# Optimization experiments

Hardware: AMD Instinct MI355X
Metric: run time of the kernel (lower is better)

## Reference

```python
import jax, jax.numpy as jnp
import numpy as np

N_NODES = 200000
N_EDGES = 5000000
N_GRAPHS = 1024
HID = 16
ALPHA = 0.2


def _sage_conv(x, src, dst, Wl, bl, Wr):
    # PyG SAGEConv(aggr='mean'): out = lin_l(mean_{j->i} x_j) + lin_r(x_i)
    msg = x[src]                                                  # [E, d] gather
    summed = jax.ops.segment_sum(msg, dst, num_segments=N_NODES)  # [N, d]
    deg = jax.ops.segment_sum(jnp.ones((src.shape[0],), x.dtype), dst, num_segments=N_NODES)
    mean = summed / jnp.maximum(deg, 1.0)[:, None]
    return mean @ Wl + bl + x @ Wr


def _attention_pool(x, batch):
    scores = jnp.exp(ALPHA * x)                                   # [N, d]
    denom = jax.ops.segment_sum(scores, batch, num_segments=N_GRAPHS)
    scores = scores / denom[batch]
    return jax.ops.segment_sum(x * scores, batch, num_segments=N_GRAPHS)  # [B, d]


def setup_inputs() -> dict:
    key = jax.random.key(0)
    ks = jax.random.split(key, 32)
    inp = {}
    inp['x'] = jax.random.normal(ks[0], (N_NODES, 1), dtype=jnp.float32)
    inp['edge_index'] = jax.random.randint(ks[1], (2, N_EDGES), 0, N_NODES, dtype=jnp.int32)
    inp['batch'] = jnp.sort(jax.random.randint(ks[2], (N_NODES,), 0, N_GRAPHS, dtype=jnp.int32))
    dims = [(1, HID), (HID, HID), (HID, HID)]
    k = 3
    for i, (di, do) in enumerate(dims):
        inp[f'Wl{i}'] = jax.random.normal(ks[k], (di, do), jnp.float32) * 0.1; k += 1
        inp[f'bl{i}'] = jnp.zeros((do,), jnp.float32)
        inp[f'Wr{i}'] = jax.random.normal(ks[k], (di, do), jnp.float32) * 0.1; k += 1
        inp[f'Wlin{i}'] = jax.random.normal(ks[k], (HID, HID), jnp.float32) * 0.1; k += 1
        inp[f'blin{i}'] = jnp.zeros((HID,), jnp.float32)
    inp['Wo0'] = jax.random.normal(ks[k], (HID, HID), jnp.float32) * 0.1; k += 1
    inp['bo0'] = jnp.zeros((HID,), jnp.float32)
    inp['Wo1'] = jax.random.normal(ks[k], (HID, HID), jnp.float32) * 0.1; k += 1
    inp['bo1'] = jnp.zeros((HID,), jnp.float32)
    inp['Wo2'] = jax.random.normal(ks[k], (HID, 1), jnp.float32) * 0.1; k += 1
    inp['bo2'] = jnp.zeros((1,), jnp.float32)
    return inp


def reference(x, edge_index, batch,
              Wl0, bl0, Wr0, Wlin0, blin0,
              Wl1, bl1, Wr1, Wlin1, blin1,
              Wl2, bl2, Wr2, Wlin2, blin2,
              Wo0, bo0, Wo1, bo1, Wo2, bo2):
    src, dst = edge_index[0], edge_index[1]
    Wls = [Wl0, Wl1, Wl2]; bls = [bl0, bl1, bl2]; Wrs = [Wr0, Wr1, Wr2]
    Wlins = [Wlin0, Wlin1, Wlin2]; blins = [blin0, blin1, blin2]
    for i in range(3):
        x = jax.nn.relu(_sage_conv(x, src, dst, Wls[i], bls[i], Wrs[i]))
        x = x @ Wlins[i] + blins[i]
    x = _attention_pool(x, batch)                                 # [B, HID]
    x = jax.nn.relu(x @ Wo0 + bo0)
    x = jax.nn.relu(x @ Wo1 + bo1)
    return x @ Wo2 + bo2                                          # [B, 1]
```

## Files before the change

kernel.cpp:

```cpp
#include <hip/hip_runtime.h>

#define N_NODES 200000
#define N_EDGES 5000000
#define N_GRAPHS 1024
#define HID 16
#define ALPHA 0.2f

#define BSH 7
#define BSZ 128
#define NB 1563
#define NWGB 256
#define EPB ((N_EDGES + NWGB - 1) / NWGB)

#define SACCP 20

__global__ void count_kernel(const int* __restrict__ dst, int* __restrict__ M) {
    __shared__ int hist[NB];
    for (int i = threadIdx.x; i < NB; i += 256) hist[i] = 0;
    __syncthreads();
    int base = blockIdx.x * EPB;
    int end = min(base + EPB, N_EDGES);
    for (int e = base + threadIdx.x; e < end; e += 256)
        atomicAdd(&hist[dst[e] >> BSH], 1);
    __syncthreads();
    for (int i = threadIdx.x; i < NB; i += 256)
        M[i * NWGB + blockIdx.x] = hist[i];
}

__global__ void colscan_kernel(int* __restrict__ M, int* __restrict__ col_total) {
    int b = blockIdx.x * blockDim.x + threadIdx.x;
    if (b >= NB) return;
    int* row = M + b * NWGB;
    int run = 0;
#pragma unroll 8
    for (int w = 0; w < NWGB; ++w) { int v = row[w]; row[w] = run; run += v; }
    col_total[b] = run;
}

__global__ void bucketscan_kernel(const int* __restrict__ col_total,
                                  int* __restrict__ bucket_base) {
    __shared__ int sc[256];
    int t = threadIdx.x;
    int v[7];
    int s = 0;
#pragma unroll
    for (int k = 0; k < 7; ++k) {
        int i = t * 7 + k;
        v[k] = (i < NB) ? col_total[i] : 0;
        s += v[k];
    }
    sc[t] = s;
    __syncthreads();
    for (int off = 1; off < 256; off <<= 1) {
        int tmp = (t >= off) ? sc[t - off] : 0;
        __syncthreads();
        sc[t] += tmp;
        __syncthreads();
    }
    int excl = sc[t] - s;
#pragma unroll
    for (int k = 0; k < 7; ++k) {
        int i = t * 7 + k;
        if (i < NB) bucket_base[i] = excl;
        excl += v[k];
    }
    if (t == 255) bucket_base[NB] = sc[255];
}

__global__ void scatter_build_kernel(const int* __restrict__ src,
                                     const int* __restrict__ dst,
                                     const int* __restrict__ M,
                                     const int* __restrict__ bucket_base,
                                     int* __restrict__ packed) {
    __shared__ int cur[NB];
    int w = blockIdx.x;
    for (int i = threadIdx.x; i < NB; i += 256)
        cur[i] = bucket_base[i] + M[i * NWGB + w];
    __syncthreads();
    int base = w * EPB;
    int end = min(base + EPB, N_EDGES);
    for (int e = base + threadIdx.x; e < end; e += 256) {
        int s = src[e], d = dst[e];
        int p = atomicAdd(&cur[d >> BSH], 1);
        packed[p] = (s << BSH) | (d & (BSZ - 1));
    }
}

__global__ void csr_kernel(const int* __restrict__ packed,
                           const int* __restrict__ bucket_base,
                           int* __restrict__ row_ptr,
                           int* __restrict__ sorted_src) {
    __shared__ int cnt[BSZ], scn[BSZ], cur[BSZ];
    int t = threadIdx.x, b = blockIdx.x;
    if (t < BSZ) cnt[t] = 0;
    __syncthreads();
    int e0 = bucket_base[b], e1 = bucket_base[b + 1];
    for (int i = e0 + t; i < e1; i += 256)
        atomicAdd(&cnt[packed[i] & (BSZ - 1)], 1);
    __syncthreads();
    if (t < BSZ) scn[t] = cnt[t];
    __syncthreads();
    for (int off = 1; off < BSZ; off <<= 1) {
        int v = 0;
        if (t < BSZ && t >= off) v = scn[t - off];
        __syncthreads();
        if (t < BSZ) scn[t] += v;
        __syncthreads();
    }
    if (t < BSZ) {
        int node = b * BSZ + t;
        int base = e0 + scn[t] - cnt[t];
        if (node < N_NODES) row_ptr[node] = base;
        cur[t] = base;
    }
    if (b == NB - 1 && t == 0) row_ptr[N_NODES] = N_EDGES;
    __syncthreads();
    for (int i = e0 + t; i < e1; i += 256) {
        int pk = packed[i];
        int p = atomicAdd(&cur[pk & (BSZ - 1)], 1);
        sorted_src[p] = pk >> BSH;
    }
}

__global__ void layer0_csr(const float* __restrict__ x,
                           const int* __restrict__ row_ptr,
                           const int* __restrict__ sorted_src,
                           const float* __restrict__ Wl, const float* __restrict__ bl,
                           const float* __restrict__ Wr,
                           const float* __restrict__ Wlin, const float* __restrict__ blin,
                           float* __restrict__ xout) {
    __shared__ float sWl[HID], sWr[HID], sbl[HID], sblin[HID], sWlin[HID * HID];
    int t = threadIdx.x;
    if (t < HID) {
        sWl[t] = Wl[t]; sWr[t] = Wr[t]; sbl[t] = bl[t]; sblin[t] = blin[t];
    }
    if (t < HID * HID) sWlin[t] = Wlin[t];
    __syncthreads();

    int n = blockIdx.x * 256 + t;
    if (n >= N_NODES) return;
    int r0 = row_ptr[n], r1 = row_ptr[n + 1];
    float sum = 0.0f;
    int i = r0;
    for (; i + 4 <= r1; i += 4) {
        int s0 = sorted_src[i], s1 = sorted_src[i + 1];
        int s2 = sorted_src[i + 2], s3 = sorted_src[i + 3];
        sum += x[s0] + x[s1] + x[s2] + x[s3];
    }
    for (; i < r1; ++i) sum += x[sorted_src[i]];
    float mean = sum / fmaxf((float)(r1 - r0), 1.0f);
    float xv = x[n];
    float h[HID];
#pragma unroll
    for (int j = 0; j < HID; ++j)
        h[j] = fmaxf(mean * sWl[j] + sbl[j] + xv * sWr[j], 0.0f);
    float o[HID];
#pragma unroll
    for (int j = 0; j < HID; ++j) {
        float a = sblin[j];
#pragma unroll
        for (int k = 0; k < HID; ++k) a += h[k] * sWlin[k * HID + j];
        o[j] = a;
    }
    float4* op = reinterpret_cast<float4*>(xout + (size_t)n * HID);
#pragma unroll
    for (int q = 0; q < 4; ++q)
        op[q] = make_float4(o[q * 4 + 0], o[q * 4 + 1], o[q * 4 + 2], o[q * 4 + 3]);
}

__global__ void layerB_csr(const float* __restrict__ xin,
                           const int* __restrict__ row_ptr,
                           const int* __restrict__ sorted_src,
                           const float* __restrict__ Wl, const float* __restrict__ bl,
                           const float* __restrict__ Wr,
                           const float* __restrict__ Wlin, const float* __restrict__ blin,
                           float* __restrict__ xout) {
    __shared__ float sacc[64 * SACCP];
    __shared__ float sxv[64 * SACCP];
    __shared__ float sh[64 * SACCP];
    __shared__ float sWl[HID * HID], sWr[HID * HID], sWlin[HID * HID];
    __shared__ float sbl[HID], sblin[HID];
    int t = threadIdx.x;
    if (t < HID * HID) { sWl[t] = Wl[t]; sWr[t] = Wr[t]; sWlin[t] = Wlin[t]; }
    if (t < HID) { sbl[t] = bl[t]; sblin[t] = blin[t]; }
    __syncthreads();

    int q = t & 3;
    int g = t >> 2;
    int n = blockIdx.x * 64 + g;

    if (n < N_NODES) {
        int r0 = row_ptr[n], r1 = row_ptr[n + 1];
        const float* xq = xin + 4 * q;
        float4 acc = make_float4(0.0f, 0.0f, 0.0f, 0.0f);
        int i = r0;
        for (; i + 4 <= r1; i += 4) {
            int s0 = sorted_src[i], s1 = sorted_src[i + 1];
            int s2 = sorted_src[i + 2], s3 = sorted_src[i + 3];
            float4 g0 = *reinterpret_cast<const float4*>(xq + (size_t)s0 * HID);
            float4 g1 = *reinterpret_cast<const float4*>(xq + (size_t)s1 * HID);
            float4 g2 = *reinterpret_cast<const float4*>(xq + (size_t)s2 * HID);
            float4 g3 = *reinterpret_cast<const float4*>(xq + (size_t)s3 * HID);
            acc.x += g0.x + g1.x + g2.x + g3.x;
            acc.y += g0.y + g1.y + g2.y + g3.y;
            acc.z += g0.z + g1.z + g2.z + g3.z;
            acc.w += g0.w + g1.w + g2.w + g3.w;
        }
        for (; i < r1; ++i) {
            float4 gv = *reinterpret_cast<const float4*>(xq + (size_t)sorted_src[i] * HID);
            acc.x += gv.x; acc.y += gv.y; acc.z += gv.z; acc.w += gv.w;
        }
        float invd = 1.0f / fmaxf((float)(r1 - r0), 1.0f);
        acc.x *= invd; acc.y *= invd; acc.z *= invd; acc.w *= invd;
        *reinterpret_cast<float4*>(&sacc[g * SACCP + 4 * q]) = acc;
        *reinterpret_cast<float4*>(&sxv[g * SACCP + 4 * q]) =
            *reinterpret_cast<const float4*>(xin + (size_t)n * HID + 4 * q);
    }
    __syncthreads();

    if (n < N_NODES) {
        float h4[4];
#pragma unroll
        for (int jj = 0; jj < 4; ++jj) {
            int j = 4 * q + jj;
            float a = sbl[j];
#pragma unroll
            for (int k = 0; k < HID; ++k)
                a += sacc[g * SACCP + k] * sWl[k * HID + j]
                   + sxv[g * SACCP + k] * sWr[k * HID + j];
            h4[jj] = fmaxf(a, 0.0f);
        }
        *reinterpret_cast<float4*>(&sh[g * SACCP + 4 * q]) =
            make_float4(h4[0], h4[1], h4[2], h4[3]);
    }
    __syncthreads();

    if (n < N_NODES) {
        float o4[4];
#pragma unroll
        for (int jj = 0; jj < 4; ++jj) {
            int j = 4 * q + jj;
            float a = sblin[j];
#pragma unroll
            for (int k = 0; k < HID; ++k) a += sh[g * SACCP + k] * sWlin[k * HID + j];
            o4[jj] = a;
        }
        *reinterpret_cast<float4*>(xout + (size_t)n * HID + 4 * q) =
            make_float4(o4[0], o4[1], o4[2], o4[3]);
    }
}

__global__ void scatter0_kernel(const float* __restrict__ x,
                                const int* __restrict__ src,
                                const int* __restrict__ dst,
                                float* __restrict__ sum0,
                                float* __restrict__ deg) {
    int stride = gridDim.x * blockDim.x;
    for (int e = blockIdx.x * blockDim.x + threadIdx.x; e < N_EDGES; e += stride) {
        atomicAdd(&sum0[dst[e]], x[src[e]]);
        atomicAdd(&deg[dst[e]], 1.0f);
    }
}

__global__ void scatter16_kernel(const float* __restrict__ x,
                                 const int* __restrict__ src,
                                 const int* __restrict__ dst,
                                 float* __restrict__ summed) {
    int stride = gridDim.x * blockDim.x;
    const int total = N_EDGES * HID;
    for (int t = blockIdx.x * blockDim.x + threadIdx.x; t < total; t += stride) {
        int e = t >> 4, j = t & 15;
        atomicAdd(&summed[dst[e] * HID + j], x[src[e] * HID + j]);
    }
}

__global__ void node0_kernel(const float* __restrict__ x,
                             const float* __restrict__ sum0,
                             const float* __restrict__ deg,
                             const float* __restrict__ Wl, const float* __restrict__ bl,
                             const float* __restrict__ Wr,
                             const float* __restrict__ Wlin, const float* __restrict__ blin,
                             float* __restrict__ xout) {
    __shared__ float sWl[HID], sWr[HID], sbl[HID], sblin[HID], sWlin[HID * HID];
    if (threadIdx.x < HID) {
        sWl[threadIdx.x] = Wl[threadIdx.x]; sWr[threadIdx.x] = Wr[threadIdx.x];
        sbl[threadIdx.x] = bl[threadIdx.x]; sblin[threadIdx.x] = blin[threadIdx.x];
    }
    if (threadIdx.x < HID * HID) sWlin[threadIdx.x] = Wlin[threadIdx.x];
    __syncthreads();
    int stride = gridDim.x * blockDim.x;
    for (int n = blockIdx.x * blockDim.x + threadIdx.x; n < N_NODES; n += stride) {
        float mean = sum0[n] / fmaxf(deg[n], 1.0f);
        float xv = x[n];
        float h[HID];
#pragma unroll
        for (int j = 0; j < HID; ++j)
            h[j] = fmaxf(mean * sWl[j] + sbl[j] + xv * sWr[j], 0.0f);
#pragma unroll
        for (int j = 0; j < HID; ++j) {
            float acc = sblin[j];
#pragma unroll
            for (int k = 0; k < HID; ++k) acc += h[k] * sWlin[k * HID + j];
            xout[n * HID + j] = acc;
        }
    }
}

__global__ void node16_kernel(const float* __restrict__ xin,
                              const float* __restrict__ sums,
                              const float* __restrict__ deg,
                              const float* __restrict__ Wl, const float* __restrict__ bl,
                              const float* __restrict__ Wr,
                              const float* __restrict__ Wlin, const float* __restrict__ blin,
                              float* __restrict__ xout) {
    __shared__ float sWl[HID * HID], sWr[HID * HID], sWlin[HID * HID];
    __shared__ float sbl[HID], sblin[HID];
    if (threadIdx.x < HID * HID) {
        sWl[threadIdx.x] = Wl[threadIdx.x]; sWr[threadIdx.x] = Wr[threadIdx.x];
        sWlin[threadIdx.x] = Wlin[threadIdx.x];
    }
    if (threadIdx.x < HID) { sbl[threadIdx.x] = bl[threadIdx.x]; sblin[threadIdx.x] = blin[threadIdx.x]; }
    __syncthreads();
    int stride = gridDim.x * blockDim.x;
    for (int n = blockIdx.x * blockDim.x + threadIdx.x; n < N_NODES; n += stride) {
        float invd = 1.0f / fmaxf(deg[n], 1.0f);
        float m[HID], xv[HID];
        const float4* sp = reinterpret_cast<const float4*>(sums + (size_t)n * HID);
        const float4* xp = reinterpret_cast<const float4*>(xin + (size_t)n * HID);
#pragma unroll
        for (int qq = 0; qq < 4; ++qq) {
            float4 sv = sp[qq]; float4 vv = xp[qq];
            m[qq * 4 + 0] = sv.x * invd; m[qq * 4 + 1] = sv.y * invd;
            m[qq * 4 + 2] = sv.z * invd; m[qq * 4 + 3] = sv.w * invd;
            xv[qq * 4 + 0] = vv.x; xv[qq * 4 + 1] = vv.y; xv[qq * 4 + 2] = vv.z; xv[qq * 4 + 3] = vv.w;
        }
        float h[HID];
#pragma unroll
        for (int j = 0; j < HID; ++j) {
            float a = sbl[j];
#pragma unroll
            for (int k = 0; k < HID; ++k) a += m[k] * sWl[k * HID + j];
#pragma unroll
            for (int k = 0; k < HID; ++k) a += xv[k] * sWr[k * HID + j];
            h[j] = fmaxf(a, 0.0f);
        }
        float o[HID];
#pragma unroll
        for (int j = 0; j < HID; ++j) {
            float a = sblin[j];
#pragma unroll
            for (int k = 0; k < HID; ++k) a += h[k] * sWlin[k * HID + j];
            o[j] = a;
        }
        float4* op = reinterpret_cast<float4*>(xout + (size_t)n * HID);
#pragma unroll
        for (int qq = 0; qq < 4; ++qq)
            op[qq] = make_float4(o[qq * 4 + 0], o[qq * 4 + 1], o[qq * 4 + 2], o[qq * 4 + 3]);
    }
}

__global__ void pool_head_kernel(const float* __restrict__ x,
                                 const int* __restrict__ batch,
                                 const float* __restrict__ Wo0, const float* __restrict__ bo0,
                                 const float* __restrict__ Wo1, const float* __restrict__ bo1,
                                 const float* __restrict__ Wo2, const float* __restrict__ bo2,
                                 float* __restrict__ out) {
    int g = blockIdx.x;
    __shared__ int sRange[2];
    __shared__ float red_d[256], red_n[256];
    __shared__ float pooled[HID], h0[HID], h1[HID];

    if (threadIdx.x == 0) {
        int lo = 0, hi = N_NODES;
        while (lo < hi) { int mid = (lo + hi) >> 1; if (batch[mid] < g) lo = mid + 1; else hi = mid; }
        sRange[0] = lo;
        hi = N_NODES;
        while (lo < hi) { int mid = (lo + hi) >> 1; if (batch[mid] < g + 1) lo = mid + 1; else hi = mid; }
        sRange[1] = lo;
    }
    __syncthreads();
    int start = sRange[0], end = sRange[1];
    int j = threadIdx.x & 15;
    int sub = threadIdx.x >> 4;

    float dacc = 0.0f, nacc = 0.0f;
    for (int n = start + sub; n < end; n += 16) {
        float v = x[n * HID + j];
        float s = expf(ALPHA * v);
        dacc += s;
        nacc += s * v;
    }
    red_d[threadIdx.x] = dacc;
    red_n[threadIdx.x] = nacc;
    __syncthreads();

    if (threadIdx.x < HID) {
        float ds = 0.0f, ns = 0.0f;
        for (int k = 0; k < 16; ++k) {
            ds += red_d[k * 16 + threadIdx.x];
            ns += red_n[k * 16 + threadIdx.x];
        }
        pooled[threadIdx.x] = ds > 0.0f ? ns / ds : 0.0f;
    }
    __syncthreads();
    if (threadIdx.x < HID) {
        float acc = bo0[threadIdx.x];
        for (int k = 0; k < HID; ++k) acc += pooled[k] * Wo0[k * HID + threadIdx.x];
        h0[threadIdx.x] = fmaxf(acc, 0.0f);
    }
    __syncthreads();
    if (threadIdx.x < HID) {
        float acc = bo1[threadIdx.x];
        for (int k = 0; k < HID; ++k) acc += h0[k] * Wo1[k * HID + threadIdx.x];
        h1[threadIdx.x] = fmaxf(acc, 0.0f);
    }
    __syncthreads();
    if (threadIdx.x == 0) {
        float acc = bo2[0];
        for (int k = 0; k < HID; ++k) acc += h1[k] * Wo2[k];
        out[g] = acc;
    }
}

extern "C" void kernel_launch(void* const* d_in, const int* in_sizes, int n_in,
                              void* d_out, int out_size, void* d_ws, size_t ws_size,
                              hipStream_t stream) {
    const float* x      = (const float*)d_in[0];
    const int*   edge   = (const int*)d_in[1];
    const int*   batch  = (const int*)d_in[2];
    const float* Wl0    = (const float*)d_in[3];
    const float* bl0    = (const float*)d_in[4];
    const float* Wr0    = (const float*)d_in[5];
    const float* Wlin0  = (const float*)d_in[6];
    const float* blin0  = (const float*)d_in[7];
    const float* Wl1    = (const float*)d_in[8];
    const float* bl1    = (const float*)d_in[9];
    const float* Wr1    = (const float*)d_in[10];
    const float* Wlin1  = (const float*)d_in[11];
    const float* blin1  = (const float*)d_in[12];
    const float* Wl2    = (const float*)d_in[13];
    const float* bl2    = (const float*)d_in[14];
    const float* Wr2    = (const float*)d_in[15];
    const float* Wlin2  = (const float*)d_in[16];
    const float* blin2  = (const float*)d_in[17];
    const float* Wo0    = (const float*)d_in[18];
    const float* bo0    = (const float*)d_in[19];
    const float* Wo1    = (const float*)d_in[20];
    const float* bo1    = (const float*)d_in[21];
    const float* Wo2    = (const float*)d_in[22];
    const float* bo2    = (const float*)d_in[23];

    const int* src = edge;
    const int* dst = edge + N_EDGES;

    const size_t OFF_SORTED = 0;
    const size_t OFF_ROW    = 20000000;
    const size_t OFF_M      = 20800016;
    const size_t OFF_XA     = 22400528;
    const size_t OFF_XB     = 35200528;
    const size_t NEED_MAIN  = 48000528;
    const size_t OFF_PACKED = OFF_XA;
    const size_t OFF_CT     = 42400528;
    const size_t OFF_BB     = 42406800;

    char* ws = (char*)d_ws;

    if (ws_size >= NEED_MAIN) {
        int*   sorted_src  = (int*)(ws + OFF_SORTED);
        int*   row_ptr     = (int*)(ws + OFF_ROW);
        int*   M           = (int*)(ws + OFF_M);
        float* xa          = (float*)(ws + OFF_XA);
        float* xb          = (float*)(ws + OFF_XB);
        int*   packed      = (int*)(ws + OFF_PACKED);
        int*   col_total   = (int*)(ws + OFF_CT);
        int*   bucket_base = (int*)(ws + OFF_BB);

        count_kernel<<<NWGB, 256, 0, stream>>>(dst, M);
        colscan_kernel<<<(NB + 255) / 256, 256, 0, stream>>>(M, col_total);
        bucketscan_kernel<<<1, 256, 0, stream>>>(col_total, bucket_base);
        scatter_build_kernel<<<NWGB, 256, 0, stream>>>(src, dst, M, bucket_base, packed);
        csr_kernel<<<NB, 256, 0, stream>>>(packed, bucket_base, row_ptr, sorted_src);

        layer0_csr<<<(N_NODES + 255) / 256, 256, 0, stream>>>(
            x, row_ptr, sorted_src, Wl0, bl0, Wr0, Wlin0, blin0, xa);
        layerB_csr<<<(N_NODES + 63) / 64, 256, 0, stream>>>(
            xa, row_ptr, sorted_src, Wl1, bl1, Wr1, Wlin1, blin1, xb);
        layerB_csr<<<(N_NODES + 63) / 64, 256, 0, stream>>>(
            xb, row_ptr, sorted_src, Wl2, bl2, Wr2, Wlin2, blin2, xa);

        pool_head_kernel<<<N_GRAPHS, 256, 0, stream>>>(xa, batch, Wo0, bo0, Wo1, bo1,
                                                       Wo2, bo2, (float*)d_out);
    } else {
        float* deg    = (float*)ws;
        float* summed = deg + N_NODES;
        float* xa     = summed + (size_t)N_NODES * HID;
        float* xb     = xa + (size_t)N_NODES * HID;

        hipMemsetAsync(deg, 0, sizeof(float) * (size_t)N_NODES * (1 + HID), stream);
        scatter0_kernel<<<2048, 256, 0, stream>>>(x, src, dst, summed, deg);
        node0_kernel<<<784, 256, 0, stream>>>(x, summed, deg, Wl0, bl0, Wr0, Wlin0, blin0, xa);

        hipMemsetAsync(summed, 0, sizeof(float) * (size_t)N_NODES * HID, stream);
        scatter16_kernel<<<4096, 256, 0, stream>>>(xa, src, dst, summed);
        node16_kernel<<<784, 256, 0, stream>>>(xa, summed, deg, Wl1, bl1, Wr1, Wlin1, blin1, xb);

        hipMemsetAsync(summed, 0, sizeof(float) * (size_t)N_NODES * HID, stream);
        scatter16_kernel<<<4096, 256, 0, stream>>>(xb, src, dst, summed);
        node16_kernel<<<784, 256, 0, stream>>>(xb, summed, deg, Wl2, bl2, Wr2, Wlin2, blin2, xa);

        pool_head_kernel<<<N_GRAPHS, 256, 0, stream>>>(xa, batch, Wo0, bo0, Wo1, bo1,
                                                       Wo2, bo2, (float*)d_out);
    }
}
```

Measured before the change: 533.8 us.

## Fuse layer-0 aggregation into CSR build and vectorize edge histogram passes

```diff
diff --git a/kernel.cpp b/kernel.cpp
--- a/kernel.cpp
+++ b/kernel.cpp
@@ -20,20 +20,28 @@
     __syncthreads();
     int base = blockIdx.x * EPB;
     int end = min(base + EPB, N_EDGES);
-    for (int e = base + threadIdx.x; e < end; e += 256)
-        atomicAdd(&hist[dst[e] >> BSH], 1);
+    for (int e = base + threadIdx.x * 4; e < end; e += 256 * 4) {
+        int4 d4 = *reinterpret_cast<const int4*>(dst + e);
+        atomicAdd(&hist[d4.x >> BSH], 1);
+        atomicAdd(&hist[d4.y >> BSH], 1);
+        atomicAdd(&hist[d4.z >> BSH], 1);
+        atomicAdd(&hist[d4.w >> BSH], 1);
+    }
     __syncthreads();
     for (int i = threadIdx.x; i < NB; i += 256)
-        M[i * NWGB + blockIdx.x] = hist[i];
+        M[blockIdx.x * NB + i] = hist[i];
 }
 
 __global__ void colscan_kernel(int* __restrict__ M, int* __restrict__ col_total) {
     int b = blockIdx.x * blockDim.x + threadIdx.x;
     if (b >= NB) return;
-    int* row = M + b * NWGB;
     int run = 0;
 #pragma unroll 8
-    for (int w = 0; w < NWGB; ++w) { int v = row[w]; row[w] = run; run += v; }
+    for (int w = 0; w < NWGB; ++w) {
+        int v = M[w * NB + b];
+        M[w * NB + b] = run;
+        run += v;
+    }
     col_total[b] = run;
 }
 
@@ -75,28 +83,40 @@
     __shared__ int cur[NB];
     int w = blockIdx.x;
     for (int i = threadIdx.x; i < NB; i += 256)
-        cur[i] = bucket_base[i] + M[i * NWGB + w];
+        cur[i] = bucket_base[i] + M[w * NB + i];
     __syncthreads();
     int base = w * EPB;
     int end = min(base + EPB, N_EDGES);
-    for (int e = base + threadIdx.x; e < end; e += 256) {
-        int s = src[e], d = dst[e];
-        int p = atomicAdd(&cur[d >> BSH], 1);
-        packed[p] = (s << BSH) | (d & (BSZ - 1));
-    }
-}
-
-__global__ void csr_kernel(const int* __restrict__ packed,
+    for (int e = base + threadIdx.x * 4; e < end; e += 256 * 4) {
+        int4 s4 = *reinterpret_cast<const int4*>(src + e);
+        int4 d4 = *reinterpret_cast<const int4*>(dst + e);
+        int p;
+        p = atomicAdd(&cur[d4.x >> BSH], 1); packed[p] = (s4.x << BSH) | (d4.x & (BSZ - 1));
+        p = atomicAdd(&cur[d4.y >> BSH], 1); packed[p] = (s4.y << BSH) | (d4.y & (BSZ - 1));
+        p = atomicAdd(&cur[d4.z >> BSH], 1); packed[p] = (s4.z << BSH) | (d4.z & (BSZ - 1));
+        p = atomicAdd(&cur[d4.w >> BSH], 1); packed[p] = (s4.w << BSH) | (d4.w & (BSZ - 1));
+    }
+}
+
+__global__ void csr_kernel(const float* __restrict__ x,
+                           const int* __restrict__ packed,
                            const int* __restrict__ bucket_base,
                            int* __restrict__ row_ptr,
-                           int* __restrict__ sorted_src) {
+                           int* __restrict__ sorted_src,
+                           float* __restrict__ sum0,
+                           float* __restrict__ degf) {
     __shared__ int cnt[BSZ], scn[BSZ], cur[BSZ];
+    __shared__ float ssum[BSZ];
     int t = threadIdx.x, b = blockIdx.x;
-    if (t < BSZ) cnt[t] = 0;
+    if (t < BSZ) { cnt[t] = 0; ssum[t] = 0.0f; }
     __syncthreads();
     int e0 = bucket_base[b], e1 = bucket_base[b + 1];
-    for (int i = e0 + t; i < e1; i += 256)
-        atomicAdd(&cnt[packed[i] & (BSZ - 1)], 1);
+    for (int i = e0 + t; i < e1; i += 256) {
+        int pk = packed[i];
+        int dl = pk & (BSZ - 1);
+        atomicAdd(&cnt[dl], 1);
+        atomicAdd(&ssum[dl], x[pk >> BSH]);
+    }
     __syncthreads();
     if (t < BSZ) scn[t] = cnt[t];
     __syncthreads();
@@ -110,7 +130,11 @@
     if (t < BSZ) {
         int node = b * BSZ + t;
         int base = e0 + scn[t] - cnt[t];
-        if (node < N_NODES) row_ptr[node] = base;
+        if (node < N_NODES) {
+            row_ptr[node] = base;
+            sum0[node] = ssum[t];
+            degf[node] = (float)cnt[t];
+        }
         cur[t] = base;
     }
     if (b == NB - 1 && t == 0) row_ptr[N_NODES] = N_EDGES;
@@ -122,50 +146,36 @@
     }
 }
 
-__global__ void layer0_csr(const float* __restrict__ x,
-                           const int* __restrict__ row_ptr,
-                           const int* __restrict__ sorted_src,
-                           const float* __restrict__ Wl, const float* __restrict__ bl,
-                           const float* __restrict__ Wr,
-                           const float* __restrict__ Wlin, const float* __restrict__ blin,
-                           float* __restrict__ xout) {
+__global__ void node0_kernel(const float* __restrict__ x,
+                             const float* __restrict__ sum0,
+                             const float* __restrict__ deg,
+                             const float* __restrict__ Wl, const float* __restrict__ bl,
+                             const float* __restrict__ Wr,
+                             const float* __restrict__ Wlin, const float* __restrict__ blin,
+                             float* __restrict__ xout) {
     __shared__ float sWl[HID], sWr[HID], sbl[HID], sblin[HID], sWlin[HID * HID];
-    int t = threadIdx.x;
-    if (t < HID) {
-        sWl[t] = Wl[t]; sWr[t] = Wr[t]; sbl[t] = bl[t]; sblin[t] = blin[t];
-    }
-    if (t < HID * HID) sWlin[t] = Wlin[t];
-    __syncthreads();
-
-    int n = blockIdx.x * 256 + t;
-    if (n >= N_NODES) return;
-    int r0 = row_ptr[n], r1 = row_ptr[n + 1];
-    float sum = 0.0f;
-    int i = r0;
-    for (; i + 4 <= r1; i += 4) {
-        int s0 = sorted_src[i], s1 = sorted_src[i + 1];
-        int s2 = sorted_src[i + 2], s3 = sorted_src[i + 3];
-        sum += x[s0] + x[s1] + x[s2] + x[s3];
-    }
-    for (; i < r1; ++i) sum += x[sorted_src[i]];
-    float mean = sum / fmaxf((float)(r1 - r0), 1.0f);
-    float xv = x[n];
-    float h[HID];
-#pragma unroll
-    for (int j = 0; j < HID; ++j)
-        h[j] = fmaxf(mean * sWl[j] + sbl[j] + xv * sWr[j], 0.0f);
-    float o[HID];
-#pragma unroll
-    for (int j = 0; j < HID; ++j) {
-        float a = sblin[j];
-#pragma unroll
-        for (int k = 0; k < HID; ++k) a += h[k] * sWlin[k * HID + j];
-        o[j] = a;
-    }
-    float4* op = reinterpret_cast<float4*>(xout + (size_t)n * HID);
-#pragma unroll
-    for (int q = 0; q < 4; ++q)
-        op[q] = make_float4(o[q * 4 + 0], o[q * 4 + 1], o[q * 4 + 2], o[q * 4 + 3]);
+    if (threadIdx.x < HID) {
+        sWl[threadIdx.x] = Wl[threadIdx.x]; sWr[threadIdx.x] = Wr[threadIdx.x];
+        sbl[threadIdx.x] = bl[threadIdx.x]; sblin[threadIdx.x] = blin[threadIdx.x];
+    }
+    if (threadIdx.x < HID * HID) sWlin[threadIdx.x] = Wlin[threadIdx.x];
+    __syncthreads();
+    int stride = gridDim.x * blockDim.x;
+    for (int n = blockIdx.x * blockDim.x + threadIdx.x; n < N_NODES; n += stride) {
+        float mean = sum0[n] / fmaxf(deg[n], 1.0f);
+        float xv = x[n];
+        float h[HID];
+#pragma unroll
+        for (int j = 0; j < HID; ++j)
+            h[j] = fmaxf(mean * sWl[j] + sbl[j] + xv * sWr[j], 0.0f);
+#pragma unroll
+        for (int j = 0; j < HID; ++j) {
+            float acc = sblin[j];
+#pragma unroll
+            for (int k = 0; k < HID; ++k) acc += h[k] * sWlin[k * HID + j];
+            xout[n * HID + j] = acc;
+        }
+    }
 }
 
 __global__ void layerB_csr(const float* __restrict__ xin,
@@ -194,8 +204,26 @@
         const float* xq = xin + 4 * q;
         float4 acc = make_float4(0.0f, 0.0f, 0.0f, 0.0f);
         int i = r0;
+        for (; i + 8 <= r1; i += 8) {
+            int s0 = sorted_src[i],     s1 = sorted_src[i + 1];
+            int s2 = sorted_src[i + 2], s3 = sorted_src[i + 3];
+            int s4 = sorted_src[i + 4], s5 = sorted_src[i + 5];
+            int s6 = sorted_src[i + 6], s7 = sorted_src[i + 7];
+            float4 g0 = *reinterpret_cast<const float4*>(xq + (size_t)s0 * HID);
+            float4 g1 = *reinterpret_cast<const float4*>(xq + (size_t)s1 * HID);
+            float4 g2 = *reinterpret_cast<const float4*>(xq + (size_t)s2 * HID);
+            float4 g3 = *reinterpret_cast<const float4*>(xq + (size_t)s3 * HID);
+            float4 g4 = *reinterpret_cast<const float4*>(xq + (size_t)s4 * HID);
+            float4 g5 = *reinterpret_cast<const float4*>(xq + (size_t)s5 * HID);
+            float4 g6 = *reinterpret_cast<const float4*>(xq + (size_t)s6 * HID);
+            float4 g7 = *reinterpret_cast<const float4*>(xq + (size_t)s7 * HID);
+            acc.x += (g0.x + g1.x + g2.x + g3.x) + (g4.x + g5.x + g6.x + g7.x);
+            acc.y += (g0.y + g1.y + g2.y + g3.y) + (g4.y + g5.y + g6.y + g7.y);
+            acc.z += (g0.z + g1.z + g2.z + g3.z) + (g4.z + g5.z + g6.z + g7.z);
+            acc.w += (g0.w + g1.w + g2.w + g3.w) + (g4.w + g5.w + g6.w + g7.w);
+        }
         for (; i + 4 <= r1; i += 4) {
-            int s0 = sorted_src[i], s1 = sorted_src[i + 1];
+            int s0 = sorted_src[i],     s1 = sorted_src[i + 1];
             int s2 = sorted_src[i + 2], s3 = sorted_src[i + 3];
             float4 g0 = *reinterpret_cast<const float4*>(xq + (size_t)s0 * HID);
             float4 g1 = *reinterpret_cast<const float4*>(xq + (size_t)s1 * HID);
@@ -271,38 +299,6 @@
     for (int t = blockIdx.x * blockDim.x + threadIdx.x; t < total; t += stride) {
         int e = t >> 4, j = t & 15;
         atomicAdd(&summed[dst[e] * HID + j], x[src[e] * HID + j]);
-    }
-}
-
-__global__ void node0_kernel(const float* __restrict__ x,
-                             const float* __restrict__ sum0,
-                             const float* __restrict__ deg,
-                             const float* __restrict__ Wl, const float* __restrict__ bl,
-                             const float* __restrict__ Wr,
-                             const float* __restrict__ Wlin, const float* __restrict__ blin,
-                             float* __restrict__ xout) {
-    __shared__ float sWl[HID], sWr[HID], sbl[HID], sblin[HID], sWlin[HID * HID];
-    if (threadIdx.x < HID) {
-        sWl[threadIdx.x] = Wl[threadIdx.x]; sWr[threadIdx.x] = Wr[threadIdx.x];
-        sbl[threadIdx.x] = bl[threadIdx.x]; sblin[threadIdx.x] = blin[threadIdx.x];
-    }
-    if (threadIdx.x < HID * HID) sWlin[threadIdx.x] = Wlin[threadIdx.x];
-    __syncthreads();
-    int stride = gridDim.x * blockDim.x;
-    for (int n = blockIdx.x * blockDim.x + threadIdx.x; n < N_NODES; n += stride) {
-        float mean = sum0[n] / fmaxf(deg[n], 1.0f);
-        float xv = x[n];
-        float h[HID];
-#pragma unroll
-        for (int j = 0; j < HID; ++j)
-            h[j] = fmaxf(mean * sWl[j] + sbl[j] + xv * sWr[j], 0.0f);
-#pragma unroll
-        for (int j = 0; j < HID; ++j) {
-            float acc = sblin[j];
-#pragma unroll
-            for (int k = 0; k < HID; ++k) acc += h[k] * sWlin[k * HID + j];
-            xout[n * HID + j] = acc;
-        }
     }
 }
 
@@ -469,6 +465,8 @@
         int*   sorted_src  = (int*)(ws + OFF_SORTED);
         int*   row_ptr     = (int*)(ws + OFF_ROW);
         int*   M           = (int*)(ws + OFF_M);
+        float* sum0        = (float*)(ws + OFF_M);
+        float* degf        = sum0 + N_NODES;
         float* xa          = (float*)(ws + OFF_XA);
         float* xb          = (float*)(ws + OFF_XB);
         int*   packed      = (int*)(ws + OFF_PACKED);
@@ -479,10 +477,10 @@
         colscan_kernel<<<(NB + 255) / 256, 256, 0, stream>>>(M, col_total);
         bucketscan_kernel<<<1, 256, 0, stream>>>(col_total, bucket_base);
         scatter_build_kernel<<<NWGB, 256, 0, stream>>>(src, dst, M, bucket_base, packed);
-        csr_kernel<<<NB, 256, 0, stream>>>(packed, bucket_base, row_ptr, sorted_src);
-
-        layer0_csr<<<(N_NODES + 255) / 256, 256, 0, stream>>>(
-            x, row_ptr, sorted_src, Wl0, bl0, Wr0, Wlin0, blin0, xa);
+        csr_kernel<<<NB, 256, 0, stream>>>(x, packed, bucket_base, row_ptr, sorted_src,
+                                           sum0, degf);
+
+        node0_kernel<<<784, 256, 0, stream>>>(x, sum0, degf, Wl0, bl0, Wr0, Wlin0, blin0, xa);
         layerB_csr<<<(N_NODES + 63) / 64, 256, 0, stream>>>(
             xa, row_ptr, sorted_src, Wl1, bl1, Wr1, Wlin1, blin1, xb);
         layerB_csr<<<(N_NODES + 63) / 64, 256, 0, stream>>>(
```

Result: slower. 652.7 us (+22.3%).

## Vectorize CSR build loads, transpose histogram layout, widen blocks, unroll gather by eight

Applied to the files above, without the earlier changes.

```diff
diff --git a/kernel.cpp b/kernel.cpp
--- a/kernel.cpp
+++ b/kernel.cpp
@@ -16,24 +16,32 @@
 
 __global__ void count_kernel(const int* __restrict__ dst, int* __restrict__ M) {
     __shared__ int hist[NB];
-    for (int i = threadIdx.x; i < NB; i += 256) hist[i] = 0;
+    for (int i = threadIdx.x; i < NB; i += 1024) hist[i] = 0;
     __syncthreads();
     int base = blockIdx.x * EPB;
     int end = min(base + EPB, N_EDGES);
-    for (int e = base + threadIdx.x; e < end; e += 256)
-        atomicAdd(&hist[dst[e] >> BSH], 1);
-    __syncthreads();
-    for (int i = threadIdx.x; i < NB; i += 256)
-        M[i * NWGB + blockIdx.x] = hist[i];
+    for (int e = base + threadIdx.x * 4; e < end; e += 1024 * 4) {
+        int4 d4 = *reinterpret_cast<const int4*>(dst + e);
+        atomicAdd(&hist[d4.x >> BSH], 1);
+        atomicAdd(&hist[d4.y >> BSH], 1);
+        atomicAdd(&hist[d4.z >> BSH], 1);
+        atomicAdd(&hist[d4.w >> BSH], 1);
+    }
+    __syncthreads();
+    for (int i = threadIdx.x; i < NB; i += 1024)
+        M[blockIdx.x * NB + i] = hist[i];
 }
 
 __global__ void colscan_kernel(int* __restrict__ M, int* __restrict__ col_total) {
     int b = blockIdx.x * blockDim.x + threadIdx.x;
     if (b >= NB) return;
-    int* row = M + b * NWGB;
     int run = 0;
 #pragma unroll 8
-    for (int w = 0; w < NWGB; ++w) { int v = row[w]; row[w] = run; run += v; }
+    for (int w = 0; w < NWGB; ++w) {
+        int v = M[w * NB + b];
+        M[w * NB + b] = run;
+        run += v;
+    }
     col_total[b] = run;
 }
 
@@ -74,15 +82,19 @@
                                      int* __restrict__ packed) {
     __shared__ int cur[NB];
     int w = blockIdx.x;
-    for (int i = threadIdx.x; i < NB; i += 256)
-        cur[i] = bucket_base[i] + M[i * NWGB + w];
+    for (int i = threadIdx.x; i < NB; i += 1024)
+        cur[i] = bucket_base[i] + M[w * NB + i];
     __syncthreads();
     int base = w * EPB;
     int end = min(base + EPB, N_EDGES);
-    for (int e = base + threadIdx.x; e < end; e += 256) {
-        int s = src[e], d = dst[e];
-        int p = atomicAdd(&cur[d >> BSH], 1);
-        packed[p] = (s << BSH) | (d & (BSZ - 1));
+    for (int e = base + threadIdx.x * 4; e < end; e += 1024 * 4) {
+        int4 s4 = *reinterpret_cast<const int4*>(src + e);
+        int4 d4 = *reinterpret_cast<const int4*>(dst + e);
+        int p;
+        p = atomicAdd(&cur[d4.x >> BSH], 1); packed[p] = (s4.x << BSH) | (d4.x & (BSZ - 1));
+        p = atomicAdd(&cur[d4.y >> BSH], 1); packed[p] = (s4.y << BSH) | (d4.y & (BSZ - 1));
+        p = atomicAdd(&cur[d4.z >> BSH], 1); packed[p] = (s4.z << BSH) | (d4.z & (BSZ - 1));
+        p = atomicAdd(&cur[d4.w >> BSH], 1); packed[p] = (s4.w << BSH) | (d4.w & (BSZ - 1));
     }
 }
 
@@ -194,8 +206,26 @@
         const float* xq = xin + 4 * q;
         float4 acc = make_float4(0.0f, 0.0f, 0.0f, 0.0f);
         int i = r0;
+        for (; i + 8 <= r1; i += 8) {
+            int s0 = sorted_src[i],     s1 = sorted_src[i + 1];
+            int s2 = sorted_src[i + 2], s3 = sorted_src[i + 3];
+            int s4 = sorted_src[i + 4], s5 = sorted_src[i + 5];
+            int s6 = sorted_src[i + 6], s7 = sorted_src[i + 7];
+            float4 g0 = *reinterpret_cast<const float4*>(xq + (size_t)s0 * HID);
+            float4 g1 = *reinterpret_cast<const float4*>(xq + (size_t)s1 * HID);
+            float4 g2 = *reinterpret_cast<const float4*>(xq + (size_t)s2 * HID);
+            float4 g3 = *reinterpret_cast<const float4*>(xq + (size_t)s3 * HID);
+            float4 g4 = *reinterpret_cast<const float4*>(xq + (size_t)s4 * HID);
+            float4 g5 = *reinterpret_cast<const float4*>(xq + (size_t)s5 * HID);
+            float4 g6 = *reinterpret_cast<const float4*>(xq + (size_t)s6 * HID);
+            float4 g7 = *reinterpret_cast<const float4*>(xq + (size_t)s7 * HID);
+            acc.x += (g0.x + g1.x + g2.x + g3.x) + (g4.x + g5.x + g6.x + g7.x);
+            acc.y += (g0.y + g1.y + g2.y + g3.y) + (g4.y + g5.y + g6.y + g7.y);
+            acc.z += (g0.z + g1.z + g2.z + g3.z) + (g4.z + g5.z + g6.z + g7.z);
+            acc.w += (g0.w + g1.w + g2.w + g3.w) + (g4.w + g5.w + g6.w + g7.w);
+        }
         for (; i + 4 <= r1; i += 4) {
-            int s0 = sorted_src[i], s1 = sorted_src[i + 1];
+            int s0 = sorted_src[i],     s1 = sorted_src[i + 1];
             int s2 = sorted_src[i + 2], s3 = sorted_src[i + 3];
             float4 g0 = *reinterpret_cast<const float4*>(xq + (size_t)s0 * HID);
             float4 g1 = *reinterpret_cast<const float4*>(xq + (size_t)s1 * HID);
@@ -475,10 +505,10 @@
         int*   col_total   = (int*)(ws + OFF_CT);
         int*   bucket_base = (int*)(ws + OFF_BB);
 
-        count_kernel<<<NWGB, 256, 0, stream>>>(dst, M);
+        count_kernel<<<NWGB, 1024, 0, stream>>>(dst, M);
         colscan_kernel<<<(NB + 255) / 256, 256, 0, stream>>>(M, col_total);
         bucketscan_kernel<<<1, 256, 0, stream>>>(col_total, bucket_base);
-        scatter_build_kernel<<<NWGB, 256, 0, stream>>>(src, dst, M, bucket_base, packed);
+        scatter_build_kernel<<<NWGB, 1024, 0, stream>>>(src, dst, M, bucket_base, packed);
         csr_kernel<<<NB, 256, 0, stream>>>(packed, bucket_base, row_ptr, sorted_src);
 
         layer0_csr<<<(N_NODES + 255) / 256, 256, 0, stream>>>(
```

New measurement: 501.1 us. -6.1%, faster.
